# Kernel optimization log

Measured on AMD Instinct MI355X. Metric: run time of the kernel, lower is better.

The kernel has to match this reference:

```python
import jax, jax.numpy as jnp
import numpy as np


def setup_inputs() -> dict:
    key = jax.random.key(0)
    k0, k1, k2, k3 = jax.random.split(key, 4)
    B, S, D, F, E = 2, 2048, 1024, 4096, 8
    scale = 0.02
    return {
        "x": jax.random.normal(k0, (B, S, D), jnp.float32),
        "gate_w": jax.random.normal(k1, (E, D), jnp.float32) * scale,
        "gate_b": jnp.zeros((E,), jnp.float32),
        "w1": jax.random.normal(k2, (E, D, F), jnp.float32) * scale,
        "b1": jnp.zeros((E, F), jnp.float32),
        "w2": jax.random.normal(k3, (E, F, D), jnp.float32) * scale,
        "b2": jnp.zeros((E, D), jnp.float32),
        "top_k": 2,
    }


def reference(x, gate_w, gate_b, w1, b1, w2, b2, top_k):
    B, S, D = x.shape
    E = gate_w.shape[0]
    xt = x.reshape(-1, D)                                   # [T, D]
    T = xt.shape[0]

    # Router: softmax over gate logits, then top-k and renormalize.
    gate_probs = jax.nn.softmax(xt @ gate_w.T + gate_b, axis=-1)   # [T, E]
    weights, selected = jax.lax.top_k(gate_probs, top_k)           # [T, k]
    weights = weights / jnp.sum(weights, axis=-1, keepdims=True)

    # Per-token combine weights over experts (zero where not selected),
    # equivalent to the per-expert gather/scatter loop in the original.
    combine = jnp.zeros((T, E), x.dtype).at[
        jnp.arange(T)[:, None], selected
    ].add(weights)                                                 # [T, E]

    # Expert MLPs (dense over experts, masked combine).
    h = jax.nn.silu(jnp.einsum("td,edf->etf", xt, w1) + b1[:, None, :])  # [E, T, F]
    expert_out = jnp.einsum("etf,efd->etd", h, w2) + b2[:, None, :]      # [E, T, D]
    out = jnp.einsum("etd,te->td", expert_out, combine)                  # [T, D]
    return out.reshape(B, S, D)
```

## Files before the change

### kernel.cpp

```cpp
#include <hip/hip_runtime.h>

#define T_TOK 4096
#define DIM   1024
#define FDIM  4096
#define NEXP  8

typedef __bf16 bf16x8 __attribute__((ext_vector_type(8)));
typedef __bf16 bf16x4 __attribute__((ext_vector_type(4)));
typedef float  f32x4  __attribute__((ext_vector_type(4)));

__device__ __forceinline__ void glds16(const void* g, void* l) {
    __builtin_amdgcn_global_load_lds(
        (const __attribute__((address_space(1))) void*)g,
        (__attribute__((address_space(3))) void*)l, 16, 0, 0);
}

__device__ __forceinline__ int xcd_swz(int phys, int total) {
    int q = total >> 3, r = total & 7;
    int x = phys & 7, i = phys >> 3;
    return (x < r ? x * (q + 1) : r * (q + 1) + (x - r) * q) + i;
}

__global__ __launch_bounds__(64)
void moe_router(const float* __restrict__ x,
                const float* __restrict__ gw,
                const float* __restrict__ gb,
                const int*   __restrict__ topk_p,
                int*   __restrict__ counts,
                int*   __restrict__ bucket,
                float* __restrict__ bweight,
                __bf16* __restrict__ xb) {
    const int t = blockIdx.x;
    const int lane = threadIdx.x;
    float part[NEXP];
#pragma unroll
    for (int e = 0; e < NEXP; ++e) part[e] = 0.f;
    const float* xrow = x + (size_t)t * DIM;
    __bf16* xbrow = xb + (size_t)t * DIM;
#pragma unroll
    for (int r = 0; r < 4; ++r) {
        int c = r * 256 + lane * 4;
        float4 v = *(const float4*)&xrow[c];
        bf16x4 o; o[0]=(__bf16)v.x; o[1]=(__bf16)v.y; o[2]=(__bf16)v.z; o[3]=(__bf16)v.w;
        *(bf16x4*)&xbrow[c] = o;
#pragma unroll
        for (int e = 0; e < NEXP; ++e) {
            float4 g = *(const float4*)&gw[e * DIM + c];
            part[e] += v.x*g.x + v.y*g.y + v.z*g.z + v.w*g.w;
        }
    }
#pragma unroll
    for (int off = 32; off > 0; off >>= 1) {
#pragma unroll
        for (int e = 0; e < NEXP; ++e) part[e] += __shfl_xor(part[e], off);
    }
    if (lane == 0) {
        int k = topk_p[0];
        if (k < 1) k = 1;
        if (k > NEXP) k = NEXP;
        float p[NEXP];
        float mx = -1e30f;
#pragma unroll
        for (int e = 0; e < NEXP; ++e) {
            p[e] = part[e] + gb[e];
            mx = fmaxf(mx, p[e]);
        }
#pragma unroll
        for (int e = 0; e < NEXP; ++e) p[e] = __expf(p[e] - mx);
        bool used[NEXP];
#pragma unroll
        for (int e = 0; e < NEXP; ++e) used[e] = false;
        int sel[NEXP]; float selp[NEXP]; float wsum = 0.f;
        for (int j = 0; j < k; ++j) {
            int best = 0; float bv = -1.f;
            for (int e = 0; e < NEXP; ++e)
                if (!used[e] && p[e] > bv) { bv = p[e]; best = e; }
            used[best] = true; sel[j] = best; selp[j] = bv; wsum += bv;
        }
        for (int j = 0; j < k; ++j) {
            int e = sel[j];
            int pos = atomicAdd(&counts[e], 1);
            bucket[e * T_TOK + pos]  = t;
            bweight[e * T_TOK + pos] = selp[j] / wsum;
        }
    }
}

__global__ __launch_bounds__(256)
void transpose_cvt(const float* __restrict__ in, __bf16* __restrict__ out,
                   int R, int C) {
    const size_t zo = (size_t)blockIdx.z * R * C;
    in += zo; out += zo;
    __shared__ float ts[64][65];
    const int c0 = blockIdx.x * 64, r0 = blockIdx.y * 64;
    const int t = threadIdx.x;
    const int rr = t >> 2, cc4 = (t & 3) * 16;
    const float* src = in + (size_t)(r0 + rr) * C + c0 + cc4;
#pragma unroll
    for (int i = 0; i < 4; ++i) {
        float4 v = *(const float4*)(src + i * 4);
        ts[rr][cc4 + i*4 + 0] = v.x; ts[rr][cc4 + i*4 + 1] = v.y;
        ts[rr][cc4 + i*4 + 2] = v.z; ts[rr][cc4 + i*4 + 3] = v.w;
    }
    __syncthreads();
    const int oc = rr, orc = cc4;
    bf16x8 o0, o1;
#pragma unroll
    for (int i = 0; i < 8; ++i) o0[i] = (__bf16)ts[orc + i][oc];
#pragma unroll
    for (int i = 0; i < 8; ++i) o1[i] = (__bf16)ts[orc + 8 + i][oc];
    __bf16* dst = out + (size_t)(c0 + oc) * R + r0 + orc;
    *(bf16x8*)dst = o0;
    *(bf16x8*)(dst + 8) = o1;
}

__global__ __launch_bounds__(64)
void build_work(const int* __restrict__ counts, int* __restrict__ hdr) {
    __shared__ int off1[NEXP + 1];
    const int lane = threadIdx.x;
    if (lane == 0) {
        int a = 0;
        for (int e = 0; e < NEXP; ++e) {
            off1[e] = a;
            a += (counts[e] + 127) >> 7;
        }
        off1[NEXP] = a;
        hdr[0] = a;
    }
    __syncthreads();
    for (int e = 0; e < NEXP; ++e) {
        int n1 = off1[e + 1] - off1[e];
        for (int j = lane; j < n1; j += 64) hdr[8 + off1[e] + j] = (e << 16) | j;
    }
}


__global__ __launch_bounds__(256, 4)
void moe_gemm1(const __bf16* __restrict__ xb,
               const __bf16* __restrict__ w1t,
               const float*  __restrict__ b1,
               const int*    __restrict__ counts,
               const int*    __restrict__ bucket,
               const int*    __restrict__ hdr,
               __bf16* __restrict__ H) {
    __shared__ __bf16 smem[16384];
    __shared__ int tok_s[128];
    const int tid = threadIdx.x;
    const int wave = tid >> 6, lane = tid & 63;
    const int wm = wave & 1, wn = wave >> 1;
    const int quad = lane >> 4, l15 = lane & 15;
    const int lrow = lane >> 2;
    const int lk8  = (lane & 3) * 8;
    char* sb = (char*)smem;
    char* dA0 = sb + wave * 2048;
    char* dA1 = sb + 8192 + wave * 2048;
    char* dB0 = sb + 16384 + wave * 2048;
    char* dB1 = sb + 24576 + wave * 2048;

    const int n1 = hdr[0];
    const int total = n1 * (FDIM / 128);
    for (int phys = blockIdx.x; phys < total; phys += gridDim.x) {
        const int u = xcd_swz(phys, total);
        const int entry = hdr[8 + (u % n1)];
        const int e = entry >> 16, tile = entry & 0xffff;
        const int nb = (u / n1) * 128;
        const int cnt = counts[e];
        if (tid < 128) {
            int r = tile * 128 + tid;
            if (r >= cnt) r = cnt - 1;
            tok_s[tid] = bucket[e * T_TOK + r];
        }
        __syncthreads();

        const int ar0 = wave * 32 + lrow;
        const __bf16* pA0 = xb + (size_t)tok_s[ar0]      * DIM + lk8;
        const __bf16* pA1 = xb + (size_t)tok_s[ar0 + 16] * DIM + lk8;
        const __bf16* pB0 = w1t + ((size_t)e * FDIM + nb + wave * 32 + lrow) * DIM + lk8;
        const __bf16* pB1 = pB0 + (size_t)16 * DIM;

        f32x4 acc[4][4];
#pragma unroll
        for (int i = 0; i < 4; ++i)
#pragma unroll
            for (int j = 0; j < 4; ++j) acc[i][j] = (f32x4){0.f,0.f,0.f,0.f};

        for (int k0 = 0; k0 < DIM; k0 += 64) {
            glds16(pA0 + k0,      dA0);
            glds16(pA0 + k0 + 32, dA1);
            glds16(pA1 + k0,      dA0 + 1024);
            glds16(pA1 + k0 + 32, dA1 + 1024);
            glds16(pB0 + k0,      dB0);
            glds16(pB0 + k0 + 32, dB1);
            glds16(pB1 + k0,      dB0 + 1024);
            glds16(pB1 + k0 + 32, dB1 + 1024);
            __syncthreads();
#pragma unroll
            for (int kk = 0; kk < 2; ++kk) {
                bf16x8 af[4], bfr[4];
#pragma unroll
                for (int i = 0; i < 4; ++i)
                    af[i] = *(const bf16x8*)&smem[kk*4096 + (wm*64 + i*16 + l15)*32 + quad*8];
#pragma unroll
                for (int j = 0; j < 4; ++j)
                    bfr[j] = *(const bf16x8*)&smem[8192 + kk*4096 + (wn*64 + j*16 + l15)*32 + quad*8];
#pragma unroll
                for (int i = 0; i < 4; ++i)
#pragma unroll
                    for (int j = 0; j < 4; ++j)
                        acc[i][j] = __builtin_amdgcn_mfma_f32_16x16x32_bf16(
                            af[i], bfr[j], acc[i][j], 0, 0, 0);
            }
            __syncthreads();
        }

        __bf16* stg = (__bf16*)(sb + wave * 2304);
        const float* b1e = b1 + e * FDIM + nb + wn * 64;
#pragma unroll
        for (int i = 0; i < 4; ++i) {
#pragma unroll
            for (int j = 0; j < 4; ++j) {
                float bias = b1e[j * 16 + l15];
#pragma unroll
                for (int r = 0; r < 4; ++r) {
                    float v = acc[i][j][r] + bias;
                    float s = v / (1.f + __expf(-v));
                    stg[(quad*4 + r) * 72 + j*16 + l15] = (__bf16)s;
                }
            }
            int prow = tile * 128 + wm * 64 + i * 16 + lrow;
            if (prow < cnt) {
                bf16x8 v0 = *(const bf16x8*)&stg[lrow * 72 + (lane & 3) * 16];
                bf16x8 v1 = *(const bf16x8*)&stg[lrow * 72 + (lane & 3) * 16 + 8];
                __bf16* dst = H + (size_t)(e * T_TOK + prow) * FDIM
                              + nb + wn * 64 + (lane & 3) * 16;
                *(bf16x8*)dst = v0;
                *(bf16x8*)(dst + 8) = v1;
            }
        }
        __syncthreads();
    }
}

#define KSPLIT 2
#define KHALF  (FDIM / KSPLIT)

__global__ __launch_bounds__(256, 4)
void moe_gemm2(const __bf16* __restrict__ H,
               const __bf16* __restrict__ w2t,
               const float*  __restrict__ b2,
               const int*    __restrict__ counts,
               const int*    __restrict__ bucket,
               const float*  __restrict__ bweight,
               const int*    __restrict__ hdr,
               float* __restrict__ out) {
    __shared__ __bf16 smem[16384];
    __shared__ int   tok_s[128];
    __shared__ float w_s[128];
    const int tid = threadIdx.x;
    const int wave = tid >> 6, lane = tid & 63;
    const int wm = wave & 1, wn = wave >> 1;
    const int quad = lane >> 4, l15 = lane & 15;
    const int lrow = lane >> 2;
    const int lk8  = (lane & 3) * 8;
    char* sb = (char*)smem;
    char* dA0 = sb + wave * 2048;
    char* dA1 = sb + 8192 + wave * 2048;
    char* dB0 = sb + 16384 + wave * 2048;
    char* dB1 = sb + 24576 + wave * 2048;

    const int n1 = hdr[0];
    const int total = n1 * (DIM / 128) * KSPLIT;
    for (int phys = blockIdx.x; phys < total; phys += gridDim.x) {
        const int u = xcd_swz(phys, total);
        const int entry = hdr[8 + (u % n1)];
        const int e = entry >> 16, tile = entry & 0xffff;
        const int rest = u / n1;
        const int nb = (rest & 7) * 128;
        const int kc = rest >> 3;
        const int cnt = counts[e];
        if (tid < 128) {
            int r  = tile * 128 + tid;
            int rc = r < cnt ? r : cnt - 1;
            tok_s[tid] = bucket[e * T_TOK + rc];
            w_s[tid]   = bweight[e * T_TOK + rc];
        }
        __syncthreads();

        const size_t kbase = (size_t)kc * KHALF;
        const __bf16* pA0 = H + (size_t)(e * T_TOK + tile * 128 + wave * 32 + lrow) * FDIM
                              + kbase + lk8;
        const __bf16* pA1 = pA0 + (size_t)16 * FDIM;
        const __bf16* pB0 = w2t + ((size_t)e * DIM + nb + wave * 32 + lrow) * FDIM
                              + kbase + lk8;
        const __bf16* pB1 = pB0 + (size_t)16 * FDIM;

        f32x4 acc[4][4];
#pragma unroll
        for (int i = 0; i < 4; ++i)
#pragma unroll
            for (int j = 0; j < 4; ++j) acc[i][j] = (f32x4){0.f,0.f,0.f,0.f};

        for (int k0 = 0; k0 < KHALF; k0 += 64) {
            glds16(pA0 + k0,      dA0);
            glds16(pA0 + k0 + 32, dA1);
            glds16(pA1 + k0,      dA0 + 1024);
            glds16(pA1 + k0 + 32, dA1 + 1024);
            glds16(pB0 + k0,      dB0);
            glds16(pB0 + k0 + 32, dB1);
            glds16(pB1 + k0,      dB0 + 1024);
            glds16(pB1 + k0 + 32, dB1 + 1024);
            __syncthreads();
#pragma unroll
            for (int kk = 0; kk < 2; ++kk) {
                bf16x8 af[4], bfr[4];
#pragma unroll
                for (int i = 0; i < 4; ++i)
                    af[i] = *(const bf16x8*)&smem[kk*4096 + (wm*64 + i*16 + l15)*32 + quad*8];
#pragma unroll
                for (int j = 0; j < 4; ++j)
                    bfr[j] = *(const bf16x8*)&smem[8192 + kk*4096 + (wn*64 + j*16 + l15)*32 + quad*8];
#pragma unroll
                for (int i = 0; i < 4; ++i)
#pragma unroll
                    for (int j = 0; j < 4; ++j)
                        acc[i][j] = __builtin_amdgcn_mfma_f32_16x16x32_bf16(
                            af[i], bfr[j], acc[i][j], 0, 0, 0);
            }
            __syncthreads();
        }

#pragma unroll
        for (int i = 0; i < 4; ++i)
#pragma unroll
            for (int j = 0; j < 4; ++j)
#pragma unroll
                for (int r = 0; r < 4; ++r) {
                    int m = wm*64 + i*16 + quad*4 + r;
                    int prow = tile * 128 + m;
                    if (prow < cnt) {
                        int dc = nb + wn*64 + j*16 + l15;
                        float v = acc[i][j][r] + (kc == 0 ? b2[e * DIM + dc] : 0.f);
                        atomicAdd(&out[(size_t)tok_s[m] * DIM + dc], w_s[m] * v);
                    }
                }
        __syncthreads();
    }
}

extern "C" void kernel_launch(void* const* d_in, const int* in_sizes, int n_in,
                              void* d_out, int out_size, void* d_ws, size_t ws_size,
                              hipStream_t stream) {
    const float* x  = (const float*)d_in[0];
    const float* gw = (const float*)d_in[1];
    const float* gb = (const float*)d_in[2];
    const float* w1 = (const float*)d_in[3];
    const float* b1 = (const float*)d_in[4];
    const float* w2 = (const float*)d_in[5];
    const float* b2 = (const float*)d_in[6];
    const int* topk = (const int*)d_in[7];
    float* out = (float*)d_out;

    char* ws = (char*)d_ws;
    size_t off = 0;
    int* counts = (int*)(ws + off);    off += 256;
    int* bucket = (int*)(ws + off);    off += (size_t)NEXP * T_TOK * 4;
    float* bw   = (float*)(ws + off);  off += (size_t)NEXP * T_TOK * 4;
    int* hdr    = (int*)(ws + off);    off += 4096;
    off = (off + 255) & ~(size_t)255;
    __bf16* xb  = (__bf16*)(ws + off); off += (size_t)T_TOK * DIM * 2;
    __bf16* w1t = (__bf16*)(ws + off); off += (size_t)NEXP * DIM * FDIM * 2;
    __bf16* w2t = (__bf16*)(ws + off); off += (size_t)NEXP * FDIM * DIM * 2;
    __bf16* H   = (__bf16*)(ws + off);

    hipMemsetAsync(counts, 0, 256, stream);
    hipMemsetAsync(out, 0, (size_t)out_size * 4, stream);

    moe_router<<<T_TOK, 64, 0, stream>>>(x, gw, gb, topk, counts, bucket, bw, xb);
    transpose_cvt<<<dim3(FDIM/64, DIM/64, NEXP), 256, 0, stream>>>(w1, w1t, DIM, FDIM);
    transpose_cvt<<<dim3(DIM/64, FDIM/64, NEXP), 256, 0, stream>>>(w2, w2t, FDIM, DIM);
    build_work<<<1, 64, 0, stream>>>(counts, hdr);

    moe_gemm1<<<2048, 256, 0, stream>>>(xb, w1t, b1, counts, bucket, hdr, H);
    moe_gemm2<<<1024, 256, 0, stream>>>(H, w2t, b2, counts, bucket, bw, hdr, out);
}
```

Before: 725.7 us.

## Use 256x256 tiles with triple-buffered swizzled LDS pipeline in MoE GEMMs

Both expert GEMMs move from 128x128 tiles with 4 waves to 256x256 tiles with 8 waves and 8x4 MFMA accumulators per wave. The K loop now uses a three-stage LDS ring with explicit vmcnt waits, so global-to-LDS loads run two steps ahead of compute. LDS rows are XOR-swizzled to avoid bank conflicts, and MFMA sections are raised to higher priority. The grids become persistent 256-block launches, and the routing work list is rebuilt with 256-row tiles. Larger tiles cut redundant weight and activation traffic but waste more rows on partially filled expert tiles and raise register and LDS pressure.

After: 833.0 us. +14.8%, slower.

```diff
diff --git a/kernel.cpp b/kernel.cpp
--- a/kernel.cpp
+++ b/kernel.cpp
@@ -122,7 +122,7 @@
         int a = 0;
         for (int e = 0; e < NEXP; ++e) {
             off1[e] = a;
-            a += (counts[e] + 127) >> 7;
+            a += (counts[e] + 255) >> 8;
         }
         off1[NEXP] = a;
         hdr[0] = a;
@@ -135,7 +135,7 @@
 }
 
 
-__global__ __launch_bounds__(256, 4)
+__global__ __launch_bounds__(512, 2)
 void moe_gemm1(const __bf16* __restrict__ xb,
                const __bf16* __restrict__ w1t,
                const float*  __restrict__ b1,
@@ -143,80 +143,103 @@
                const int*    __restrict__ bucket,
                const int*    __restrict__ hdr,
                __bf16* __restrict__ H) {
-    __shared__ __bf16 smem[16384];
-    __shared__ int tok_s[128];
+    __shared__ __align__(16) char sb[3 * 32768];
+    __shared__ int tok_s[256];
     const int tid = threadIdx.x;
     const int wave = tid >> 6, lane = tid & 63;
     const int wm = wave & 1, wn = wave >> 1;
     const int quad = lane >> 4, l15 = lane & 15;
     const int lrow = lane >> 2;
-    const int lk8  = (lane & 3) * 8;
-    char* sb = (char*)smem;
-    char* dA0 = sb + wave * 2048;
-    char* dA1 = sb + 8192 + wave * 2048;
-    char* dB0 = sb + 16384 + wave * 2048;
-    char* dB1 = sb + 24576 + wave * 2048;
-
+    const int rr  = tid >> 2;
+    const int srh = ((tid & 3) ^ ((tid >> 3) & 3)) * 8;
+    const int swz16 = (((lane >> 4) ^ ((lane >> 1) & 3)) << 4);
+    const int aoff = (wm * 128 + l15) * 64 + swz16;
+    const int boff = (wn * 64  + l15) * 64 + swz16;
+
+    const int NT = DIM / 32;
     const int n1 = hdr[0];
-    const int total = n1 * (FDIM / 128);
+    const int total = n1 * (FDIM / 256);
     for (int phys = blockIdx.x; phys < total; phys += gridDim.x) {
         const int u = xcd_swz(phys, total);
         const int entry = hdr[8 + (u % n1)];
         const int e = entry >> 16, tile = entry & 0xffff;
-        const int nb = (u / n1) * 128;
+        const int nb = (u / n1) * 256;
         const int cnt = counts[e];
-        if (tid < 128) {
-            int r = tile * 128 + tid;
-            if (r >= cnt) r = cnt - 1;
-            tok_s[tid] = bucket[e * T_TOK + r];
+        for (int r = tid; r < 256; r += 512) {
+            int rw = tile * 256 + r;
+            if (rw >= cnt) rw = cnt - 1;
+            tok_s[r] = bucket[e * T_TOK + rw];
         }
         __syncthreads();
 
-        const int ar0 = wave * 32 + lrow;
-        const __bf16* pA0 = xb + (size_t)tok_s[ar0]      * DIM + lk8;
-        const __bf16* pA1 = xb + (size_t)tok_s[ar0 + 16] * DIM + lk8;
-        const __bf16* pB0 = w1t + ((size_t)e * FDIM + nb + wave * 32 + lrow) * DIM + lk8;
-        const __bf16* pB1 = pB0 + (size_t)16 * DIM;
-
-        f32x4 acc[4][4];
-#pragma unroll
-        for (int i = 0; i < 4; ++i)
+        const __bf16* pa0 = xb + (size_t)tok_s[rr]       * DIM + srh;
+        const __bf16* pa1 = xb + (size_t)tok_s[rr + 128] * DIM + srh;
+        const __bf16* pb0 = w1t + ((size_t)e * FDIM + nb + rr) * DIM + srh;
+        const __bf16* pb1 = pb0 + (size_t)128 * DIM;
+
+        f32x4 acc[8][4];
+#pragma unroll
+        for (int i = 0; i < 8; ++i)
 #pragma unroll
             for (int j = 0; j < 4; ++j) acc[i][j] = (f32x4){0.f,0.f,0.f,0.f};
 
-        for (int k0 = 0; k0 < DIM; k0 += 64) {
-            glds16(pA0 + k0,      dA0);
-            glds16(pA0 + k0 + 32, dA1);
-            glds16(pA1 + k0,      dA0 + 1024);
-            glds16(pA1 + k0 + 32, dA1 + 1024);
-            glds16(pB0 + k0,      dB0);
-            glds16(pB0 + k0 + 32, dB1);
-            glds16(pB1 + k0,      dB0 + 1024);
-            glds16(pB1 + k0 + 32, dB1 + 1024);
-            __syncthreads();
-#pragma unroll
-            for (int kk = 0; kk < 2; ++kk) {
-                bf16x8 af[4], bfr[4];
-#pragma unroll
-                for (int i = 0; i < 4; ++i)
-                    af[i] = *(const bf16x8*)&smem[kk*4096 + (wm*64 + i*16 + l15)*32 + quad*8];
+#pragma unroll
+        for (int p = 0; p < 2; ++p) {
+            char* db = sb + p * 32768;
+            const int ko = p * 32;
+            glds16(pa0 + ko, db + wave * 1024);
+            glds16(pa1 + ko, db + 8192 + wave * 1024);
+            glds16(pb0 + ko, db + 16384 + wave * 1024);
+            glds16(pb1 + ko, db + 24576 + wave * 1024);
+        }
+
+        int bc = 0, bn = 2;
+#pragma unroll 1
+        for (int t = 0; t < NT; ++t) {
+            if (t + 2 < NT) {
+                char* db = sb + bn * 32768;
+                const int ko = (t + 2) * 32;
+                glds16(pa0 + ko, db + wave * 1024);
+                glds16(pa1 + ko, db + 8192 + wave * 1024);
+                glds16(pb0 + ko, db + 16384 + wave * 1024);
+                glds16(pb1 + ko, db + 24576 + wave * 1024);
+                asm volatile("s_waitcnt vmcnt(8)" ::: "memory");
+            } else if (t + 2 == NT) {
+                asm volatile("s_waitcnt vmcnt(4)" ::: "memory");
+            } else {
+                asm volatile("s_waitcnt vmcnt(0)" ::: "memory");
+            }
+            __builtin_amdgcn_s_barrier();
+            asm volatile("" ::: "memory");
+
+            const char* Ab = sb + bc * 32768;
+            const char* Bb = Ab + 16384;
+            bf16x8 af[8], bfr[4];
+#pragma unroll
+            for (int i = 0; i < 8; ++i)
+                af[i] = *(const bf16x8*)(Ab + aoff + i * 1024);
+#pragma unroll
+            for (int j = 0; j < 4; ++j)
+                bfr[j] = *(const bf16x8*)(Bb + boff + j * 1024);
+            __builtin_amdgcn_s_setprio(1);
+#pragma unroll
+            for (int i = 0; i < 8; ++i)
 #pragma unroll
                 for (int j = 0; j < 4; ++j)
-                    bfr[j] = *(const bf16x8*)&smem[8192 + kk*4096 + (wn*64 + j*16 + l15)*32 + quad*8];
-#pragma unroll
-                for (int i = 0; i < 4; ++i)
-#pragma unroll
-                    for (int j = 0; j < 4; ++j)
-                        acc[i][j] = __builtin_amdgcn_mfma_f32_16x16x32_bf16(
-                            af[i], bfr[j], acc[i][j], 0, 0, 0);
-            }
-            __syncthreads();
+                    acc[i][j] = __builtin_amdgcn_mfma_f32_16x16x32_bf16(
+                        af[i], bfr[j], acc[i][j], 0, 0, 0);
+            __builtin_amdgcn_s_setprio(0);
+
+            asm volatile("" ::: "memory");
+            __builtin_amdgcn_s_barrier();
+            bc = (bc == 2) ? 0 : bc + 1;
+            bn = (bn == 2) ? 0 : bn + 1;
         }
 
         __bf16* stg = (__bf16*)(sb + wave * 2304);
         const float* b1e = b1 + e * FDIM + nb + wn * 64;
 #pragma unroll
-        for (int i = 0; i < 4; ++i) {
+        for (int i = 0; i < 8; ++i) {
 #pragma unroll
             for (int j = 0; j < 4; ++j) {
                 float bias = b1e[j * 16 + l15];
@@ -227,7 +250,7 @@
                     stg[(quad*4 + r) * 72 + j*16 + l15] = (__bf16)s;
                 }
             }
-            int prow = tile * 128 + wm * 64 + i * 16 + lrow;
+            int prow = tile * 256 + wm * 128 + i * 16 + lrow;
             if (prow < cnt) {
                 bf16x8 v0 = *(const bf16x8*)&stg[lrow * 72 + (lane & 3) * 16];
                 bf16x8 v1 = *(const bf16x8*)&stg[lrow * 72 + (lane & 3) * 16 + 8];
@@ -244,7 +267,7 @@
 #define KSPLIT 2
 #define KHALF  (FDIM / KSPLIT)
 
-__global__ __launch_bounds__(256, 4)
+__global__ __launch_bounds__(512, 2)
 void moe_gemm2(const __bf16* __restrict__ H,
                const __bf16* __restrict__ w2t,
                const float*  __restrict__ b2,
@@ -253,93 +276,118 @@
                const float*  __restrict__ bweight,
                const int*    __restrict__ hdr,
                float* __restrict__ out) {
-    __shared__ __bf16 smem[16384];
-    __shared__ int   tok_s[128];
-    __shared__ float w_s[128];
+    __shared__ __align__(16) char sb[3 * 32768];
+    __shared__ int   tok_s[256];
+    __shared__ float w_s[256];
     const int tid = threadIdx.x;
     const int wave = tid >> 6, lane = tid & 63;
     const int wm = wave & 1, wn = wave >> 1;
     const int quad = lane >> 4, l15 = lane & 15;
-    const int lrow = lane >> 2;
-    const int lk8  = (lane & 3) * 8;
-    char* sb = (char*)smem;
-    char* dA0 = sb + wave * 2048;
-    char* dA1 = sb + 8192 + wave * 2048;
-    char* dB0 = sb + 16384 + wave * 2048;
-    char* dB1 = sb + 24576 + wave * 2048;
-
+    const int rr  = tid >> 2;
+    const int srh = ((tid & 3) ^ ((tid >> 3) & 3)) * 8;
+    const int swz16 = (((lane >> 4) ^ ((lane >> 1) & 3)) << 4);
+    const int aoff = (wm * 128 + l15) * 64 + swz16;
+    const int boff = (wn * 64  + l15) * 64 + swz16;
+
+    const int NT = KHALF / 32;
     const int n1 = hdr[0];
-    const int total = n1 * (DIM / 128) * KSPLIT;
+    const int total = n1 * (DIM / 256) * KSPLIT;
     for (int phys = blockIdx.x; phys < total; phys += gridDim.x) {
         const int u = xcd_swz(phys, total);
         const int entry = hdr[8 + (u % n1)];
         const int e = entry >> 16, tile = entry & 0xffff;
         const int rest = u / n1;
-        const int nb = (rest & 7) * 128;
-        const int kc = rest >> 3;
+        const int nb = (rest & 3) * 256;
+        const int kc = rest >> 2;
         const int cnt = counts[e];
-        if (tid < 128) {
-            int r  = tile * 128 + tid;
-            int rc = r < cnt ? r : cnt - 1;
-            tok_s[tid] = bucket[e * T_TOK + rc];
-            w_s[tid]   = bweight[e * T_TOK + rc];
+        for (int r = tid; r < 256; r += 512) {
+            int rw = tile * 256 + r;
+            int rc = rw < cnt ? rw : cnt - 1;
+            tok_s[r] = bucket[e * T_TOK + rc];
+            w_s[r]   = bweight[e * T_TOK + rc];
         }
         __syncthreads();
 
         const size_t kbase = (size_t)kc * KHALF;
-        const __bf16* pA0 = H + (size_t)(e * T_TOK + tile * 128 + wave * 32 + lrow) * FDIM
-                              + kbase + lk8;
-        const __bf16* pA1 = pA0 + (size_t)16 * FDIM;
-        const __bf16* pB0 = w2t + ((size_t)e * DIM + nb + wave * 32 + lrow) * FDIM
-                              + kbase + lk8;
-        const __bf16* pB1 = pB0 + (size_t)16 * FDIM;
-
-        f32x4 acc[4][4];
-#pragma unroll
-        for (int i = 0; i < 4; ++i)
+        const __bf16* pa0 = H + (size_t)(e * T_TOK + tile * 256 + rr) * FDIM + kbase + srh;
+        const __bf16* pa1 = pa0 + (size_t)128 * FDIM;
+        const __bf16* pb0 = w2t + ((size_t)e * DIM + nb + rr) * FDIM + kbase + srh;
+        const __bf16* pb1 = pb0 + (size_t)128 * FDIM;
+
+        f32x4 acc[8][4];
+#pragma unroll
+        for (int i = 0; i < 8; ++i)
 #pragma unroll
             for (int j = 0; j < 4; ++j) acc[i][j] = (f32x4){0.f,0.f,0.f,0.f};
 
-        for (int k0 = 0; k0 < KHALF; k0 += 64) {
-            glds16(pA0 + k0,      dA0);
-            glds16(pA0 + k0 + 32, dA1);
-            glds16(pA1 + k0,      dA0 + 1024);
-            glds16(pA1 + k0 + 32, dA1 + 1024);
-            glds16(pB0 + k0,      dB0);
-            glds16(pB0 + k0 + 32, dB1);
-            glds16(pB1 + k0,      dB0 + 1024);
-            glds16(pB1 + k0 + 32, dB1 + 1024);
-            __syncthreads();
-#pragma unroll
-            for (int kk = 0; kk < 2; ++kk) {
-                bf16x8 af[4], bfr[4];
-#pragma unroll
-                for (int i = 0; i < 4; ++i)
-                    af[i] = *(const bf16x8*)&smem[kk*4096 + (wm*64 + i*16 + l15)*32 + quad*8];
+#pragma unroll
+        for (int p = 0; p < 2; ++p) {
+            char* db = sb + p * 32768;
+            const int ko = p * 32;
+            glds16(pa0 + ko, db + wave * 1024);
+            glds16(pa1 + ko, db + 8192 + wave * 1024);
+            glds16(pb0 + ko, db + 16384 + wave * 1024);
+            glds16(pb1 + ko, db + 24576 + wave * 1024);
+        }
+
+        int bc = 0, bn = 2;
+#pragma unroll 1
+        for (int t = 0; t < NT; ++t) {
+            if (t + 2 < NT) {
+                char* db = sb + bn * 32768;
+                const int ko = (t + 2) * 32;
+                glds16(pa0 + ko, db + wave * 1024);
+                glds16(pa1 + ko, db + 8192 + wave * 1024);
+                glds16(pb0 + ko, db + 16384 + wave * 1024);
+                glds16(pb1 + ko, db + 24576 + wave * 1024);
+                asm volatile("s_waitcnt vmcnt(8)" ::: "memory");
+            } else if (t + 2 == NT) {
+                asm volatile("s_waitcnt vmcnt(4)" ::: "memory");
+            } else {
+                asm volatile("s_waitcnt vmcnt(0)" ::: "memory");
+            }
+            __builtin_amdgcn_s_barrier();
+            asm volatile("" ::: "memory");
+
+            const char* Ab = sb + bc * 32768;
+            const char* Bb = Ab + 16384;
+            bf16x8 af[8], bfr[4];
+#pragma unroll
+            for (int i = 0; i < 8; ++i)
+                af[i] = *(const bf16x8*)(Ab + aoff + i * 1024);
+#pragma unroll
+            for (int j = 0; j < 4; ++j)
+                bfr[j] = *(const bf16x8*)(Bb + boff + j * 1024);
+            __builtin_amdgcn_s_setprio(1);
+#pragma unroll
+            for (int i = 0; i < 8; ++i)
 #pragma unroll
                 for (int j = 0; j < 4; ++j)
-                    bfr[j] = *(const bf16x8*)&smem[8192 + kk*4096 + (wn*64 + j*16 + l15)*32 + quad*8];
-#pragma unroll
-                for (int i = 0; i < 4; ++i)
-#pragma unroll
-                    for (int j = 0; j < 4; ++j)
-                        acc[i][j] = __builtin_amdgcn_mfma_f32_16x16x32_bf16(
-                            af[i], bfr[j], acc[i][j], 0, 0, 0);
-            }
-            __syncthreads();
-        }
-
-#pragma unroll
-        for (int i = 0; i < 4; ++i)
+                    acc[i][j] = __builtin_amdgcn_mfma_f32_16x16x32_bf16(
+                        af[i], bfr[j], acc[i][j], 0, 0, 0);
+            __builtin_amdgcn_s_setprio(0);
+
+            asm volatile("" ::: "memory");
+            __builtin_amdgcn_s_barrier();
+            bc = (bc == 2) ? 0 : bc + 1;
+            bn = (bn == 2) ? 0 : bn + 1;
+        }
+
+        float bias[4];
+#pragma unroll
+        for (int j = 0; j < 4; ++j)
+            bias[j] = (kc == 0) ? b2[e * DIM + nb + wn * 64 + j * 16 + l15] : 0.f;
+#pragma unroll
+        for (int i = 0; i < 8; ++i)
 #pragma unroll
             for (int j = 0; j < 4; ++j)
 #pragma unroll
                 for (int r = 0; r < 4; ++r) {
-                    int m = wm*64 + i*16 + quad*4 + r;
-                    int prow = tile * 128 + m;
+                    int m = wm * 128 + i * 16 + quad * 4 + r;
+                    int prow = tile * 256 + m;
                     if (prow < cnt) {
-                        int dc = nb + wn*64 + j*16 + l15;
-                        float v = acc[i][j][r] + (kc == 0 ? b2[e * DIM + dc] : 0.f);
+                        int dc = nb + wn * 64 + j * 16 + l15;
+                        float v = acc[i][j][r] + bias[j];
                         atomicAdd(&out[(size_t)tok_s[m] * DIM + dc], w_s[m] * v);
                     }
                 }
@@ -380,6 +428,6 @@
     transpose_cvt<<<dim3(DIM/64, FDIM/64, NEXP), 256, 0, stream>>>(w2, w2t, FDIM, DIM);
     build_work<<<1, 64, 0, stream>>>(counts, hdr);
 
-    moe_gemm1<<<2048, 256, 0, stream>>>(xb, w1t, b1, counts, bucket, hdr, H);
-    moe_gemm2<<<1024, 256, 0, stream>>>(H, w2t, b2, counts, bucket, bw, hdr, out);
-}
+    moe_gemm1<<<256, 512, 0, stream>>>(xb, w1t, b1, counts, bucket, hdr, H);
+    moe_gemm2<<<256, 512, 0, stream>>>(H, w2t, b2, counts, bucket, bw, hdr, out);
+}
```

## Enlarge MoE GEMM tiles to 256x256 with pipelined swizzled LDS and gather-combine

Applied to the files above, without the earlier changes.

Both expert GEMMs move to 512-thread blocks computing 256x256 tiles. They double-buffer global-to-LDS loads with an XOR swizzle, issue hand-scheduled ds_read_b128 reads under raised wave priority, and wait on explicit vmcnt/lgkmcnt counts. The second GEMM no longer does scattered float atomicAdds into the output. It writes bf16 partial results per K-split into padded per-expert row buffers, and a new combine kernel gathers each token's top-k rows and applies the routing weights. This trades the atomic traffic and the output memset for an extra kernel, more workspace, and bf16 rounding of the intermediate expert outputs.

After: 847.0 us. 1.17x slower.

```diff
diff --git a/kernel.cpp b/kernel.cpp
--- a/kernel.cpp
+++ b/kernel.cpp
@@ -4,16 +4,21 @@
 #define DIM   1024
 #define FDIM  4096
 #define NEXP  8
+#define PADROWS 10240
 
 typedef __bf16 bf16x8 __attribute__((ext_vector_type(8)));
 typedef __bf16 bf16x4 __attribute__((ext_vector_type(4)));
 typedef float  f32x4  __attribute__((ext_vector_type(4)));
+typedef const __attribute__((address_space(3))) char* lds3;
 
 __device__ __forceinline__ void glds16(const void* g, void* l) {
     __builtin_amdgcn_global_load_lds(
         (const __attribute__((address_space(1))) void*)g,
         (__attribute__((address_space(3))) void*)l, 16, 0, 0);
 }
+
+#define DSR(dst, a, imm) \
+    asm volatile("ds_read_b128 %0, %1 offset:" #imm : "=v"(dst) : "v"(a))
 
 __device__ __forceinline__ int xcd_swz(int phys, int total) {
     int q = total >> 3, r = total & 7;
@@ -28,7 +33,8 @@
                 const int*   __restrict__ topk_p,
                 int*   __restrict__ counts,
                 int*   __restrict__ bucket,
-                float* __restrict__ bweight,
+                int*   __restrict__ slot,
+                float* __restrict__ tw,
                 __bf16* __restrict__ xb) {
     const int t = blockIdx.x;
     const int lane = threadIdx.x;
@@ -80,8 +86,9 @@
         for (int j = 0; j < k; ++j) {
             int e = sel[j];
             int pos = atomicAdd(&counts[e], 1);
-            bucket[e * T_TOK + pos]  = t;
-            bweight[e * T_TOK + pos] = selp[j] / wsum;
+            bucket[e * T_TOK + pos] = t;
+            slot[t * 8 + j] = (e << 12) | pos;
+            tw[t * 8 + j]   = selp[j] / wsum;
         }
     }
 }
@@ -119,10 +126,13 @@
     __shared__ int off1[NEXP + 1];
     const int lane = threadIdx.x;
     if (lane == 0) {
-        int a = 0;
+        int a = 0, rows = 0;
         for (int e = 0; e < NEXP; ++e) {
             off1[e] = a;
-            a += (counts[e] + 127) >> 7;
+            hdr[16 + e] = rows;
+            int nt = (counts[e] + 255) >> 8;
+            a += nt;
+            rows += nt * 256;
         }
         off1[NEXP] = a;
         hdr[0] = a;
@@ -130,12 +140,73 @@
     __syncthreads();
     for (int e = 0; e < NEXP; ++e) {
         int n1 = off1[e + 1] - off1[e];
-        for (int j = lane; j < n1; j += 64) hdr[8 + off1[e] + j] = (e << 16) | j;
-    }
-}
-
-
-__global__ __launch_bounds__(256, 4)
+        for (int j = lane; j < n1; j += 64) hdr[32 + off1[e] + j] = (e << 16) | j;
+    }
+}
+
+#define MFMA_CL(AF, BF) do { \
+    _Pragma("unroll") for (int i_ = 0; i_ < 8; ++i_) \
+    _Pragma("unroll") for (int j_ = 0; j_ < 4; ++j_) \
+        acc[i_][j_] = __builtin_amdgcn_mfma_f32_16x16x32_bf16( \
+            AF[i_], BF[j_], acc[i_][j_], 0, 0, 0); } while (0)
+
+#define WINBODY(A0, A1, B0, B1) do { \
+    bf16x8 af[8], b0r[4], b1r[4]; \
+    DSR(af[0],(A0),0);    DSR(af[1],(A0),2048); \
+    DSR(af[2],(A0),4096); DSR(af[3],(A0),6144); \
+    DSR(af[4],(A0),8192); DSR(af[5],(A0),10240); \
+    DSR(af[6],(A0),12288);DSR(af[7],(A0),14336); \
+    DSR(b0r[0],(B0),0);   DSR(b0r[1],(B0),2048); \
+    DSR(b0r[2],(B0),4096);DSR(b0r[3],(B0),6144); \
+    DSR(b1r[0],(B1),0);   DSR(b1r[1],(B1),2048); \
+    DSR(b1r[2],(B1),4096);DSR(b1r[3],(B1),6144); \
+    asm volatile("s_waitcnt lgkmcnt(4)"); \
+    __builtin_amdgcn_sched_barrier(0); \
+    __builtin_amdgcn_s_setprio(1); \
+    MFMA_CL(af, b0r); \
+    __builtin_amdgcn_s_setprio(0); \
+    __builtin_amdgcn_sched_barrier(0); \
+    DSR(af[0],(A1),0);    DSR(af[1],(A1),2048); \
+    DSR(af[2],(A1),4096); DSR(af[3],(A1),6144); \
+    DSR(af[4],(A1),8192); DSR(af[5],(A1),10240); \
+    DSR(af[6],(A1),12288);DSR(af[7],(A1),14336); \
+    asm volatile("s_waitcnt lgkmcnt(0)"); \
+    __builtin_amdgcn_sched_barrier(0); \
+    __builtin_amdgcn_s_setprio(1); \
+    MFMA_CL(af, b1r); \
+    __builtin_amdgcn_s_setprio(0); \
+    __builtin_amdgcn_sched_barrier(0); } while (0)
+
+#define STAGE8(DST, PA, PB, KO) do { \
+    glds16(PA[0]+(KO), (DST));         glds16(PA[1]+(KO), (DST)+8192); \
+    glds16(PA[2]+(KO), (DST)+16384);   glds16(PA[3]+(KO), (DST)+24576); \
+    glds16(PB[0]+(KO), (DST)+32768);   glds16(PB[1]+(KO), (DST)+40960); \
+    glds16(PB[2]+(KO), (DST)+49152);   glds16(PB[3]+(KO), (DST)+57344); } while (0)
+
+#define KLOOP(NW) do { \
+    STAGE8(st0, pa, pb, 0); \
+    for (int tw_ = 0; tw_ < (NW); tw_ += 2) { \
+        STAGE8(st1, pa, pb, (tw_ + 1) * 64); \
+        __builtin_amdgcn_sched_barrier(0); \
+        asm volatile("s_waitcnt vmcnt(8)"); \
+        __builtin_amdgcn_sched_barrier(0); \
+        __builtin_amdgcn_s_barrier(); \
+        WINBODY(rA00, rA01, rB00, rB01); \
+        __builtin_amdgcn_s_barrier(); \
+        if (tw_ + 2 < (NW)) { \
+            STAGE8(st0, pa, pb, (tw_ + 2) * 64); \
+            __builtin_amdgcn_sched_barrier(0); \
+            asm volatile("s_waitcnt vmcnt(8)"); \
+        } else { \
+            asm volatile("s_waitcnt vmcnt(0)"); \
+        } \
+        __builtin_amdgcn_sched_barrier(0); \
+        __builtin_amdgcn_s_barrier(); \
+        WINBODY(rA10, rA11, rB10, rB11); \
+        __builtin_amdgcn_s_barrier(); \
+    } } while (0)
+
+__global__ __launch_bounds__(512, 2)
 void moe_gemm1(const __bf16* __restrict__ xb,
                const __bf16* __restrict__ w1t,
                const float*  __restrict__ b1,
@@ -143,80 +214,63 @@
                const int*    __restrict__ bucket,
                const int*    __restrict__ hdr,
                __bf16* __restrict__ H) {
-    __shared__ __bf16 smem[16384];
-    __shared__ int tok_s[128];
+    __shared__ __align__(16) char sb[2 * 65536];
+    __shared__ int tok_s[256];
     const int tid = threadIdx.x;
     const int wave = tid >> 6, lane = tid & 63;
     const int wm = wave & 1, wn = wave >> 1;
     const int quad = lane >> 4, l15 = lane & 15;
     const int lrow = lane >> 2;
-    const int lk8  = (lane & 3) * 8;
-    char* sb = (char*)smem;
-    char* dA0 = sb + wave * 2048;
-    char* dA1 = sb + 8192 + wave * 2048;
-    char* dB0 = sb + 16384 + wave * 2048;
-    char* dB1 = sb + 24576 + wave * 2048;
+    const int srcoff = ((lane & 7) ^ ((lane >> 3) & 7)) * 8;
+    char* st0 = sb + wave * 1024;
+    char* st1 = sb + 65536 + wave * 1024;
+    lds3 s3 = (lds3)sb;
+    const int arow = (wm * 128 + l15) * 128;
+    const int brow = 32768 + (wn * 64 + l15) * 128;
+    const int ch0 = ((quad     ^ (l15 & 7)) << 4);
+    const int ch1 = (((4+quad) ^ (l15 & 7)) << 4);
+    lds3 rA00 = s3 + arow + ch0,          rA01 = s3 + arow + ch1;
+    lds3 rB00 = s3 + brow + ch0,          rB01 = s3 + brow + ch1;
+    lds3 rA10 = rA00 + 65536,             rA11 = rA01 + 65536;
+    lds3 rB10 = rB00 + 65536,             rB11 = rB01 + 65536;
 
     const int n1 = hdr[0];
-    const int total = n1 * (FDIM / 128);
+    const int total = n1 * (FDIM / 256);
     for (int phys = blockIdx.x; phys < total; phys += gridDim.x) {
         const int u = xcd_swz(phys, total);
-        const int entry = hdr[8 + (u % n1)];
+        const int entry = hdr[32 + (u % n1)];
         const int e = entry >> 16, tile = entry & 0xffff;
-        const int nb = (u / n1) * 128;
+        const int nb = (u / n1) * 256;
         const int cnt = counts[e];
-        if (tid < 128) {
-            int r = tile * 128 + tid;
-            if (r >= cnt) r = cnt - 1;
-            tok_s[tid] = bucket[e * T_TOK + r];
+        const int grow0 = hdr[16 + e] + tile * 256;
+        if (tid < 256) {
+            int rw = tile * 256 + tid;
+            if (rw >= cnt) rw = cnt - 1;
+            tok_s[tid] = bucket[e * T_TOK + rw];
         }
         __syncthreads();
 
-        const int ar0 = wave * 32 + lrow;
-        const __bf16* pA0 = xb + (size_t)tok_s[ar0]      * DIM + lk8;
-        const __bf16* pA1 = xb + (size_t)tok_s[ar0 + 16] * DIM + lk8;
-        const __bf16* pB0 = w1t + ((size_t)e * FDIM + nb + wave * 32 + lrow) * DIM + lk8;
-        const __bf16* pB1 = pB0 + (size_t)16 * DIM;
-
-        f32x4 acc[4][4];
-#pragma unroll
-        for (int i = 0; i < 4; ++i)
+        const __bf16* pa[4];
+        const __bf16* pb[4];
+#pragma unroll
+        for (int q = 0; q < 4; ++q) {
+            int rq = q * 64 + wave * 8 + (lane >> 3);
+            pa[q] = xb + (size_t)tok_s[rq] * DIM + srcoff;
+            pb[q] = w1t + ((size_t)e * FDIM + nb + rq) * DIM + srcoff;
+        }
+
+        f32x4 acc[8][4];
+#pragma unroll
+        for (int i = 0; i < 8; ++i)
 #pragma unroll
             for (int j = 0; j < 4; ++j) acc[i][j] = (f32x4){0.f,0.f,0.f,0.f};
 
-        for (int k0 = 0; k0 < DIM; k0 += 64) {
-            glds16(pA0 + k0,      dA0);
-            glds16(pA0 + k0 + 32, dA1);
-            glds16(pA1 + k0,      dA0 + 1024);
-            glds16(pA1 + k0 + 32, dA1 + 1024);
-            glds16(pB0 + k0,      dB0);
-            glds16(pB0 + k0 + 32, dB1);
-            glds16(pB1 + k0,      dB0 + 1024);
-            glds16(pB1 + k0 + 32, dB1 + 1024);
-            __syncthreads();
-#pragma unroll
-            for (int kk = 0; kk < 2; ++kk) {
-                bf16x8 af[4], bfr[4];
-#pragma unroll
-                for (int i = 0; i < 4; ++i)
-                    af[i] = *(const bf16x8*)&smem[kk*4096 + (wm*64 + i*16 + l15)*32 + quad*8];
-#pragma unroll
-                for (int j = 0; j < 4; ++j)
-                    bfr[j] = *(const bf16x8*)&smem[8192 + kk*4096 + (wn*64 + j*16 + l15)*32 + quad*8];
-#pragma unroll
-                for (int i = 0; i < 4; ++i)
-#pragma unroll
-                    for (int j = 0; j < 4; ++j)
-                        acc[i][j] = __builtin_amdgcn_mfma_f32_16x16x32_bf16(
-                            af[i], bfr[j], acc[i][j], 0, 0, 0);
-            }
-            __syncthreads();
-        }
+        KLOOP(16);
 
         __bf16* stg = (__bf16*)(sb + wave * 2304);
         const float* b1e = b1 + e * FDIM + nb + wn * 64;
 #pragma unroll
-        for (int i = 0; i < 4; ++i) {
+        for (int i = 0; i < 8; ++i) {
 #pragma unroll
             for (int j = 0; j < 4; ++j) {
                 float bias = b1e[j * 16 + l15];
@@ -227,15 +281,12 @@
                     stg[(quad*4 + r) * 72 + j*16 + l15] = (__bf16)s;
                 }
             }
-            int prow = tile * 128 + wm * 64 + i * 16 + lrow;
-            if (prow < cnt) {
-                bf16x8 v0 = *(const bf16x8*)&stg[lrow * 72 + (lane & 3) * 16];
-                bf16x8 v1 = *(const bf16x8*)&stg[lrow * 72 + (lane & 3) * 16 + 8];
-                __bf16* dst = H + (size_t)(e * T_TOK + prow) * FDIM
-                              + nb + wn * 64 + (lane & 3) * 16;
-                *(bf16x8*)dst = v0;
-                *(bf16x8*)(dst + 8) = v1;
-            }
+            int grow = grow0 + wm * 128 + i * 16 + lrow;
+            bf16x8 v0 = *(const bf16x8*)&stg[lrow * 72 + (lane & 3) * 16];
+            bf16x8 v1 = *(const bf16x8*)&stg[lrow * 72 + (lane & 3) * 16 + 8];
+            __bf16* dst = H + (size_t)grow * FDIM + nb + wn * 64 + (lane & 3) * 16;
+            *(bf16x8*)dst = v0;
+            *(bf16x8*)(dst + 8) = v1;
         }
         __syncthreads();
     }
@@ -244,107 +295,116 @@
 #define KSPLIT 2
 #define KHALF  (FDIM / KSPLIT)
 
-__global__ __launch_bounds__(256, 4)
+__global__ __launch_bounds__(512, 2)
 void moe_gemm2(const __bf16* __restrict__ H,
                const __bf16* __restrict__ w2t,
                const float*  __restrict__ b2,
-               const int*    __restrict__ counts,
-               const int*    __restrict__ bucket,
-               const float*  __restrict__ bweight,
                const int*    __restrict__ hdr,
-               float* __restrict__ out) {
-    __shared__ __bf16 smem[16384];
-    __shared__ int   tok_s[128];
-    __shared__ float w_s[128];
+               __bf16* __restrict__ Y0,
+               __bf16* __restrict__ Y1) {
+    __shared__ __align__(16) char sb[2 * 65536];
     const int tid = threadIdx.x;
     const int wave = tid >> 6, lane = tid & 63;
     const int wm = wave & 1, wn = wave >> 1;
     const int quad = lane >> 4, l15 = lane & 15;
     const int lrow = lane >> 2;
-    const int lk8  = (lane & 3) * 8;
-    char* sb = (char*)smem;
-    char* dA0 = sb + wave * 2048;
-    char* dA1 = sb + 8192 + wave * 2048;
-    char* dB0 = sb + 16384 + wave * 2048;
-    char* dB1 = sb + 24576 + wave * 2048;
+    const int srcoff = ((lane & 7) ^ ((lane >> 3) & 7)) * 8;
+    char* st0 = sb + wave * 1024;
+    char* st1 = sb + 65536 + wave * 1024;
+    lds3 s3 = (lds3)sb;
+    const int arow = (wm * 128 + l15) * 128;
+    const int brow = 32768 + (wn * 64 + l15) * 128;
+    const int ch0 = ((quad     ^ (l15 & 7)) << 4);
+    const int ch1 = (((4+quad) ^ (l15 & 7)) << 4);
+    lds3 rA00 = s3 + arow + ch0,          rA01 = s3 + arow + ch1;
+    lds3 rB00 = s3 + brow + ch0,          rB01 = s3 + brow + ch1;
+    lds3 rA10 = rA00 + 65536,             rA11 = rA01 + 65536;
+    lds3 rB10 = rB00 + 65536,             rB11 = rB01 + 65536;
 
     const int n1 = hdr[0];
-    const int total = n1 * (DIM / 128) * KSPLIT;
+    const int total = n1 * (DIM / 256) * KSPLIT;
     for (int phys = blockIdx.x; phys < total; phys += gridDim.x) {
         const int u = xcd_swz(phys, total);
-        const int entry = hdr[8 + (u % n1)];
+        const int entry = hdr[32 + (u % n1)];
         const int e = entry >> 16, tile = entry & 0xffff;
         const int rest = u / n1;
-        const int nb = (rest & 7) * 128;
-        const int kc = rest >> 3;
-        const int cnt = counts[e];
-        if (tid < 128) {
-            int r  = tile * 128 + tid;
-            int rc = r < cnt ? r : cnt - 1;
-            tok_s[tid] = bucket[e * T_TOK + rc];
-            w_s[tid]   = bweight[e * T_TOK + rc];
-        }
+        const int nb = (rest & 3) * 256;
+        const int kc = rest >> 2;
+        const int grow0 = hdr[16 + e] + tile * 256;
+        const size_t kbase = (size_t)kc * KHALF;
+
+        const __bf16* pa[4];
+        const __bf16* pb[4];
+#pragma unroll
+        for (int q = 0; q < 4; ++q) {
+            int rq = q * 64 + wave * 8 + (lane >> 3);
+            pa[q] = H + (size_t)(grow0 + rq) * FDIM + kbase + srcoff;
+            pb[q] = w2t + ((size_t)e * DIM + nb + rq) * FDIM + kbase + srcoff;
+        }
+
+        f32x4 acc[8][4];
+#pragma unroll
+        for (int i = 0; i < 8; ++i)
+#pragma unroll
+            for (int j = 0; j < 4; ++j) acc[i][j] = (f32x4){0.f,0.f,0.f,0.f};
+
         __syncthreads();
 
-        const size_t kbase = (size_t)kc * KHALF;
-        const __bf16* pA0 = H + (size_t)(e * T_TOK + tile * 128 + wave * 32 + lrow) * FDIM
-                              + kbase + lk8;
-        const __bf16* pA1 = pA0 + (size_t)16 * FDIM;
-        const __bf16* pB0 = w2t + ((size_t)e * DIM + nb + wave * 32 + lrow) * FDIM
-                              + kbase + lk8;
-        const __bf16* pB1 = pB0 + (size_t)16 * FDIM;
-
-        f32x4 acc[4][4];
-#pragma unroll
-        for (int i = 0; i < 4; ++i)
-#pragma unroll
-            for (int j = 0; j < 4; ++j) acc[i][j] = (f32x4){0.f,0.f,0.f,0.f};
-
-        for (int k0 = 0; k0 < KHALF; k0 += 64) {
-            glds16(pA0 + k0,      dA0);
-            glds16(pA0 + k0 + 32, dA1);
-            glds16(pA1 + k0,      dA0 + 1024);
-            glds16(pA1 + k0 + 32, dA1 + 1024);
-            glds16(pB0 + k0,      dB0);
-            glds16(pB0 + k0 + 32, dB1);
-            glds16(pB1 + k0,      dB0 + 1024);
-            glds16(pB1 + k0 + 32, dB1 + 1024);
-            __syncthreads();
-#pragma unroll
-            for (int kk = 0; kk < 2; ++kk) {
-                bf16x8 af[4], bfr[4];
-#pragma unroll
-                for (int i = 0; i < 4; ++i)
-                    af[i] = *(const bf16x8*)&smem[kk*4096 + (wm*64 + i*16 + l15)*32 + quad*8];
-#pragma unroll
-                for (int j = 0; j < 4; ++j)
-                    bfr[j] = *(const bf16x8*)&smem[8192 + kk*4096 + (wn*64 + j*16 + l15)*32 + quad*8];
-#pragma unroll
-                for (int i = 0; i < 4; ++i)
-#pragma unroll
-                    for (int j = 0; j < 4; ++j)
-                        acc[i][j] = __builtin_amdgcn_mfma_f32_16x16x32_bf16(
-                            af[i], bfr[j], acc[i][j], 0, 0, 0);
+        KLOOP(32);
+
+        __bf16* Y = kc == 0 ? Y0 : Y1;
+        __bf16* stg = (__bf16*)(sb + wave * 2304);
+        const float* b2e = b2 + e * DIM + nb + wn * 64;
+#pragma unroll
+        for (int i = 0; i < 8; ++i) {
+#pragma unroll
+            for (int j = 0; j < 4; ++j) {
+                float bias = (kc == 0) ? b2e[j * 16 + l15] : 0.f;
+#pragma unroll
+                for (int r = 0; r < 4; ++r) {
+                    float v = acc[i][j][r] + bias;
+                    stg[(quad*4 + r) * 72 + j*16 + l15] = (__bf16)v;
+                }
             }
-            __syncthreads();
-        }
-
-#pragma unroll
-        for (int i = 0; i < 4; ++i)
-#pragma unroll
-            for (int j = 0; j < 4; ++j)
-#pragma unroll
-                for (int r = 0; r < 4; ++r) {
-                    int m = wm*64 + i*16 + quad*4 + r;
-                    int prow = tile * 128 + m;
-                    if (prow < cnt) {
-                        int dc = nb + wn*64 + j*16 + l15;
-                        float v = acc[i][j][r] + (kc == 0 ? b2[e * DIM + dc] : 0.f);
-                        atomicAdd(&out[(size_t)tok_s[m] * DIM + dc], w_s[m] * v);
-                    }
-                }
+            int grow = grow0 + wm * 128 + i * 16 + lrow;
+            bf16x8 v0 = *(const bf16x8*)&stg[lrow * 72 + (lane & 3) * 16];
+            bf16x8 v1 = *(const bf16x8*)&stg[lrow * 72 + (lane & 3) * 16 + 8];
+            __bf16* dst = Y + (size_t)grow * DIM + nb + wn * 64 + (lane & 3) * 16;
+            *(bf16x8*)dst = v0;
+            *(bf16x8*)(dst + 8) = v1;
+        }
         __syncthreads();
     }
+}
+
+__global__ __launch_bounds__(256)
+void moe_combine(const __bf16* __restrict__ Y0,
+                 const __bf16* __restrict__ Y1,
+                 const int*    __restrict__ slot,
+                 const float*  __restrict__ tw,
+                 const int*    __restrict__ topk_p,
+                 const int*    __restrict__ hdr,
+                 float* __restrict__ out) {
+    const int t = blockIdx.x;
+    const int c = threadIdx.x * 4;
+    int k = topk_p[0];
+    if (k < 1) k = 1;
+    if (k > NEXP) k = NEXP;
+    float a0 = 0.f, a1 = 0.f, a2 = 0.f, a3 = 0.f;
+    for (int j = 0; j < k; ++j) {
+        int s = slot[t * 8 + j];
+        int e = s >> 12, pos = s & 4095;
+        int g = hdr[16 + e] + pos;
+        float w = tw[t * 8 + j];
+        bf16x4 y0 = *(const bf16x4*)&Y0[(size_t)g * DIM + c];
+        bf16x4 y1 = *(const bf16x4*)&Y1[(size_t)g * DIM + c];
+        a0 += w * ((float)y0[0] + (float)y1[0]);
+        a1 += w * ((float)y0[1] + (float)y1[1]);
+        a2 += w * ((float)y0[2] + (float)y1[2]);
+        a3 += w * ((float)y0[3] + (float)y1[3]);
+    }
+    float4 o = {a0, a1, a2, a3};
+    *(float4*)&out[(size_t)t * DIM + c] = o;
 }
 
 extern "C" void kernel_launch(void* const* d_in, const int* in_sizes, int n_in,
@@ -364,22 +424,25 @@
     size_t off = 0;
     int* counts = (int*)(ws + off);    off += 256;
     int* bucket = (int*)(ws + off);    off += (size_t)NEXP * T_TOK * 4;
-    float* bw   = (float*)(ws + off);  off += (size_t)NEXP * T_TOK * 4;
+    int* slot   = (int*)(ws + off);    off += (size_t)T_TOK * 8 * 4;
+    float* tw   = (float*)(ws + off);  off += (size_t)T_TOK * 8 * 4;
     int* hdr    = (int*)(ws + off);    off += 4096;
     off = (off + 255) & ~(size_t)255;
     __bf16* xb  = (__bf16*)(ws + off); off += (size_t)T_TOK * DIM * 2;
     __bf16* w1t = (__bf16*)(ws + off); off += (size_t)NEXP * DIM * FDIM * 2;
     __bf16* w2t = (__bf16*)(ws + off); off += (size_t)NEXP * FDIM * DIM * 2;
-    __bf16* H   = (__bf16*)(ws + off);
+    __bf16* H   = (__bf16*)(ws + off); off += (size_t)PADROWS * FDIM * 2;
+    __bf16* Y0  = (__bf16*)(ws + off); off += (size_t)PADROWS * DIM * 2;
+    __bf16* Y1  = (__bf16*)(ws + off);
 
     hipMemsetAsync(counts, 0, 256, stream);
-    hipMemsetAsync(out, 0, (size_t)out_size * 4, stream);
-
-    moe_router<<<T_TOK, 64, 0, stream>>>(x, gw, gb, topk, counts, bucket, bw, xb);
+
+    moe_router<<<T_TOK, 64, 0, stream>>>(x, gw, gb, topk, counts, bucket, slot, tw, xb);
     transpose_cvt<<<dim3(FDIM/64, DIM/64, NEXP), 256, 0, stream>>>(w1, w1t, DIM, FDIM);
     transpose_cvt<<<dim3(DIM/64, FDIM/64, NEXP), 256, 0, stream>>>(w2, w2t, FDIM, DIM);
     build_work<<<1, 64, 0, stream>>>(counts, hdr);
 
-    moe_gemm1<<<2048, 256, 0, stream>>>(xb, w1t, b1, counts, bucket, hdr, H);
-    moe_gemm2<<<1024, 256, 0, stream>>>(H, w2t, b2, counts, bucket, bw, hdr, out);
-}
+    moe_gemm1<<<512, 512, 0, stream>>>(xb, w1t, b1, counts, bucket, hdr, H);
+    moe_gemm2<<<512, 512, 0, stream>>>(H, w2t, b2, hdr, Y0, Y1);
+    moe_combine<<<T_TOK, 256, 0, stream>>>(Y0, Y1, slot, tw, topk, hdr, out);
+}
```
